# Optimization experiments

Hardware: AMD Instinct MI355X
Metric: run time of the kernel (lower is better)

The kernel has to match this reference:

```python
import jax, jax.numpy as jnp
import numpy as np

B, C, W, F, NC = 512, 12, 4, 512, 4  # batch, leads, windows(=4, hardcoded by conv0), features, classes


def setup_inputs() -> dict:
    key = jax.random.key(0)
    ks = jax.random.split(key, 16)
    g = lambda i, shape, s=1.0: jax.random.normal(ks[i], shape, jnp.float32) * s
    return {
        "x": g(0, (B, C, W, F)),
        # GRU (PyTorch layout: W_ih [3F,F], W_hh [3F,F], gate order r,z,n)
        "gru_wih": g(1, (3 * F, F), 0.03),
        "gru_whh": g(2, (3 * F, F), 0.03),
        "gru_bih": jnp.zeros((3 * F,), jnp.float32),
        "gru_bhh": jnp.zeros((3 * F,), jnp.float32),
        # GraphLearning 1x1 convs (squeezed kernels); positive biases keep adj nondegenerate
        "conv0_w": g(3, (W,), 0.5), "conv0_b": jnp.float32(0.1),
        "conv1_w": g(4, (F,), 0.05), "conv1_b": jnp.float32(0.1),
        "conv2_w": g(5, (C * C, C), 0.3),
        "conv2_b": 0.1 + 0.05 * jnp.abs(g(6, (C * C,))),
        # GCN stack
        "gcn_w": g(7, (2, F, F), 0.04), "gcn_b": jnp.zeros((2, F), jnp.float32),
        # classifier head (jax [in,out] layout); BN in eval mode
        "fc1_w": g(8, (C * F, 512), 0.02), "fc1_b": jnp.zeros((512,), jnp.float32),
        "bn1_g": jnp.ones((512,), jnp.float32), "bn1_b": jnp.zeros((512,), jnp.float32),
        "bn1_m": 0.1 * g(9, (512,)), "bn1_v": 1.0 + 0.1 * jnp.abs(g(10, (512,))),
        "fc2_w": g(11, (512, 512), 0.04), "fc2_b": jnp.zeros((512,), jnp.float32),
        "bn2_g": jnp.ones((512,), jnp.float32), "bn2_b": jnp.zeros((512,), jnp.float32),
        "bn2_m": 0.1 * g(12, (512,)), "bn2_v": 1.0 + 0.1 * jnp.abs(g(13, (512,))),
        "fc3_w": g(14, (512, NC), 0.04), "fc3_b": jnp.zeros((NC,), jnp.float32),
    }


def reference(x, gru_wih, gru_whh, gru_bih, gru_bhh,
              conv0_w, conv0_b, conv1_w, conv1_b, conv2_w, conv2_b,
              gcn_w, gcn_b,
              fc1_w, fc1_b, bn1_g, bn1_b, bn1_m, bn1_v,
              fc2_w, fc2_b, bn2_g, bn2_b, bn2_m, bn2_v,
              fc3_w, fc3_b):
    b, c, w, f = x.shape
    # --- GRU over leads dim; each window slice starts from h0=0, so merge (batch, w) ---
    xs = x.transpose(0, 2, 1, 3).reshape(b * w, c, f)            # [N, C, F]
    xW = jnp.einsum('ntf,gf->ntg', xs, gru_wih) + gru_bih        # precompute input gates [N,C,3F]

    def step(h, xw_t):
        hg = h @ gru_whh.T + gru_bhh
        xr, xz, xn = jnp.split(xw_t, 3, axis=-1)
        hr, hz, hn = jnp.split(hg, 3, axis=-1)
        r = jax.nn.sigmoid(xr + hr)
        z = jax.nn.sigmoid(xz + hz)
        n = jnp.tanh(xn + r * hn)
        h = (1.0 - z) * n + z * h
        return h, h

    _, hs = jax.lax.scan(step, jnp.zeros((b * w, f), x.dtype), xW.transpose(1, 0, 2))
    gru_out = hs.transpose(1, 0, 2).reshape(b, w, c, f).transpose(0, 2, 1, 3)  # [B,C,W,F]

    # --- GraphLearning: 1x1 convs -> 12x12 adjacency -> normalized Laplacian -> Chebyshev K=4 ---
    g0 = gru_out.transpose(0, 2, 1, 3)                               # [B,W,C,F]
    y = jax.nn.relu(jnp.einsum('bwcf,w->bcf', g0, conv0_w) + conv0_b)  # [B,C,F]
    y = jax.nn.relu(jnp.einsum('bcf,f->bc', y, conv1_w) + conv1_b)     # [B,C]
    y = jax.nn.relu(jnp.einsum('bc,kc->bk', y, conv2_w) + conv2_b)     # [B,C*C]
    a = jnp.mean(y.reshape(b, c, c), axis=0)
    adj = jax.nn.relu(a)
    degree = jnp.sum(adj, axis=1)
    adj_s = 0.5 * (adj + adj.T)
    d_hat = 1.0 / (jnp.sqrt(degree) + 1e-7)
    lap = d_hat[:, None] * (jnp.diag(degree) - adj_s) * d_hat[None, :]
    L0 = jnp.zeros_like(lap)
    L1 = lap
    L2 = 2.0 * lap @ L1 - L0
    L3 = 2.0 * lap @ L2 - L1
    cheb = jnp.stack([L0, L1, L2, L3], axis=0)                       # [4,C,C]

    # --- GCN stack with residuals (dropout is identity in eval) ---
    h = gru_out.transpose(0, 2, 1, 3)[:, :, None]                    # [B,W,1,C,F]
    tmp = h
    res = h
    for i in range(gcn_w.shape[0]):
        support = jnp.einsum('bwocf,fg->bwocg', h, gcn_w[i])
        out = jnp.einsum('wij,bwojf->bwoif', cheb, support) + gcn_b[i]
        h = jax.nn.relu(out) + res
        res = h
    h = tmp + h
    h = h[:, :, 0].sum(1).reshape(b, c * f)                          # [B, C*F]

    # --- classifier head (eval-mode BN, dropout identity) ---
    def bn(v, gmm, bt, m, var):
        return (v - m) / jnp.sqrt(var + 1e-5) * gmm + bt

    h = bn(jax.nn.leaky_relu(h @ fc1_w + fc1_b, 0.01), bn1_g, bn1_b, bn1_m, bn1_v)
    h = bn(jax.nn.leaky_relu(h @ fc2_w + fc2_b, 0.01), bn2_g, bn2_b, bn2_m, bn2_v)
    return h @ fc3_w + fc3_b
```

## Files before the change

### kernel.cpp

```cpp
#include <hip/hip_runtime.h>
#include <cmath>

constexpr int Bb  = 512;
constexpr int Cc  = 12;
constexpr int Ww  = 4;
constexpr int Ff  = 512;
constexpr int Nn  = Bb * Ww;
constexpr int Gg  = 3 * Ff;
constexpr int Mx  = Nn * Cc;

typedef __attribute__((ext_vector_type(8))) short bf16x8;
typedef __attribute__((ext_vector_type(4))) float f32x4;

__device__ __forceinline__ float sigm(float v) { return 1.f / (1.f + expf(-v)); }
__device__ __forceinline__ float b2f(ushort u) { union { float f; unsigned i; } v; v.i = ((unsigned)u) << 16; return v.f; }
__device__ __forceinline__ ushort f2b(float f) {
    union { float f; unsigned i; } v; v.f = f;
    unsigned r = v.i + 0x7FFFu + ((v.i >> 16) & 1u);
    return (ushort)(r >> 16);
}
__device__ __forceinline__ void async16(const ushort* g, ushort* l) {
    __builtin_amdgcn_global_load_lds(
        (const __attribute__((address_space(1))) unsigned int*)g,
        (__attribute__((address_space(3))) unsigned int*)l, 16, 0, 0);
}

__global__ __launch_bounds__(256) void mfma_gemm(
    const ushort* __restrict__ A, const ushort* __restrict__ Bt,
    float* __restrict__ Cf, ushort* __restrict__ Cb,
    const float* __restrict__ colBias,
    int N, int K, int kLen, int MN, int gridY)
{
    __shared__ ushort As[128 * 64], Bs[128 * 64];
    const int tid = threadIdx.x;
    const int ln = tid & 63, wv = tid >> 6;
    const int l = blockIdx.x;
    const int by = l % gridY, bx = l / gridY, bz = blockIdx.y;
    const int srow = ln >> 3;
    const int kslot = (ln & 7) ^ srow;
    const int rowA0 = by * 128 + wv * 32;
    const int rowB0 = bx * 128 + wv * 32;
    const ushort* ga = A  + (long)(rowA0 + srow) * K + bz * kLen + kslot * 8;
    const ushort* gb = Bt + (long)(rowB0 + srow) * K + bz * kLen + kslot * 8;
    ushort* la = As + wv * 32 * 64;
    ushort* lb = Bs + wv * 32 * 64;
    const int rbase = (wv >> 1) * 64, cbase = (wv & 1) * 64;
    const int mrow = ln & 15, quad = ln >> 4;

    f32x4 acc[4][4] = {};

    for (int kc = 0; kc < kLen; kc += 64) {
        #pragma unroll
        for (int i = 0; i < 4; ++i) {
            async16(ga + (long)(i * 8) * K, la + i * 8 * 64);
            async16(gb + (long)(i * 8) * K, lb + i * 8 * 64);
        }
        ga += 64; gb += 64;
        __syncthreads();
        #pragma unroll
        for (int s = 0; s < 2; ++s) {
            const int sw = (((s << 2) + quad) ^ (ln & 7)) << 3;
            bf16x8 af[4], bf[4];
            #pragma unroll
            for (int i = 0; i < 4; ++i)
                af[i] = *(const bf16x8*)(As + (rbase + i * 16 + mrow) * 64 + sw);
            #pragma unroll
            for (int j = 0; j < 4; ++j)
                bf[j] = *(const bf16x8*)(Bs + (cbase + j * 16 + mrow) * 64 + sw);
            #pragma unroll
            for (int i = 0; i < 4; ++i)
                #pragma unroll
                for (int j = 0; j < 4; ++j)
                    acc[i][j] = __builtin_amdgcn_mfma_f32_16x16x32_bf16(bf[j], af[i], acc[i][j], 0, 0, 0);
        }
        __syncthreads();
    }

    const int gr0 = by * 128 + rbase + mrow;
    const int gc0 = bx * 128 + cbase + quad * 4;
    if (Cb) {
        #pragma unroll
        for (int i = 0; i < 4; ++i) {
            const long rowoff = (long)(gr0 + i * 16) * N;
            #pragma unroll
            for (int j = 0; j < 4; ++j) {
                float c0 = 0.f, c1 = 0.f, c2 = 0.f, c3 = 0.f;
                if (colBias) {
                    const float4 cb4 = *(const float4*)(colBias + gc0 + j * 16);
                    c0 = cb4.x; c1 = cb4.y; c2 = cb4.z; c3 = cb4.w;
                }
                union { ushort u[4]; uint2 v; } pk;
                pk.u[0] = f2b(acc[i][j][0] + c0);
                pk.u[1] = f2b(acc[i][j][1] + c1);
                pk.u[2] = f2b(acc[i][j][2] + c2);
                pk.u[3] = f2b(acc[i][j][3] + c3);
                *(uint2*)&Cb[rowoff + gc0 + j * 16] = pk.v;
            }
        }
    } else {
        float* Co = Cf + (long)bz * MN;
        #pragma unroll
        for (int i = 0; i < 4; ++i) {
            const long rowoff = (long)(gr0 + i * 16) * N;
            #pragma unroll
            for (int j = 0; j < 4; ++j)
                *(f32x4*)&Co[rowoff + gc0 + j * 16] = acc[i][j];
        }
    }
}

__global__ __launch_bounds__(256) void gru_fused(
    const ushort* __restrict__ hin, const ushort* __restrict__ xb,
    const ushort* __restrict__ whhB, const ushort* __restrict__ wihB,
    const float* __restrict__ bih, const float* __restrict__ bhh,
    ushort* __restrict__ hout, ushort* __restrict__ G, int t)
{
    __shared__ ushort Ah[64 * 64], Ax[64 * 64], Bh[96 * 64], Bx[96 * 64];
    const int tid = threadIdx.x, ln = tid & 63, wv = tid >> 6;
    const int mb = blockIdx.x & 31, fb = blockIdx.x >> 5;
    const int srow = ln >> 3, kslot = (ln & 7) ^ srow;
    const int mrow = ln & 15, quad = ln >> 4;
    f32x4 aH[6] = {}, aX[6] = {};
    const ushort* hrow = hin + (long)(mb * 64) * 512;

    for (int kc = 0; kc < 512; kc += 64) {
        #pragma unroll
        for (int a = 0; a < 2; ++a) {
            const int r0 = (wv * 2 + a) * 8;
            async16(hrow + (long)(r0 + srow) * 512 + kc + kslot * 8, Ah + r0 * 64);
            async16(xb + ((long)(mb * 64 + r0 + srow) * 12 + t) * 512 + kc + kslot * 8, Ax + r0 * 64);
        }
        #pragma unroll
        for (int b8 = 0; b8 < 3; ++b8) {
            const int lr0 = (wv * 3 + b8) * 8;
            const int lr = lr0 + srow;
            const int g = lr >> 5, fc = lr & 31;
            const long wr = (long)(g * 512 + fb * 32 + fc) * 512 + kc + kslot * 8;
            async16(whhB + wr, Bh + lr0 * 64);
            async16(wihB + wr, Bx + lr0 * 64);
        }
        __syncthreads();
        #pragma unroll
        for (int s = 0; s < 2; ++s) {
            const int sw = (((s << 2) + quad) ^ (ln & 7)) << 3;
            const bf16x8 ah = *(const bf16x8*)(Ah + (wv * 16 + mrow) * 64 + sw);
            const bf16x8 ax = *(const bf16x8*)(Ax + (wv * 16 + mrow) * 64 + sw);
            #pragma unroll
            for (int jt = 0; jt < 6; ++jt) {
                const bf16x8 bh = *(const bf16x8*)(Bh + (jt * 16 + mrow) * 64 + sw);
                aH[jt] = __builtin_amdgcn_mfma_f32_16x16x32_bf16(bh, ah, aH[jt], 0, 0, 0);
            }
            #pragma unroll
            for (int jt = 0; jt < 6; ++jt) {
                const bf16x8 bx2 = *(const bf16x8*)(Bx + (jt * 16 + mrow) * 64 + sw);
                aX[jt] = __builtin_amdgcn_mfma_f32_16x16x32_bf16(bx2, ax, aX[jt], 0, 0, 0);
            }
        }
        __syncthreads();
    }

    const int n = mb * 64 + wv * 16 + mrow;
    #pragma unroll
    for (int ft = 0; ft < 2; ++ft) {
        const int f0 = fb * 32 + ft * 16 + quad * 4;
        const float4 bir = *(const float4*)(bih + f0);
        const float4 biz = *(const float4*)(bih + 512 + f0);
        const float4 bin = *(const float4*)(bih + 1024 + f0);
        const float4 bhr = *(const float4*)(bhh + f0);
        const float4 bhz = *(const float4*)(bhh + 512 + f0);
        const float4 bhn = *(const float4*)(bhh + 1024 + f0);
        union { ushort u[4]; uint2 v; } hp;
        hp.v = *(const uint2*)(hin + (long)n * 512 + f0);
        const float br[4] = {bir.x + bhr.x, bir.y + bhr.y, bir.z + bhr.z, bir.w + bhr.w};
        const float bz[4] = {biz.x + bhz.x, biz.y + bhz.y, biz.z + bhz.z, biz.w + bhz.w};
        const float bn_i[4] = {bin.x, bin.y, bin.z, bin.w};
        const float bn_h[4] = {bhn.x, bhn.y, bhn.z, bhn.w};
        union { ushort u[4]; uint2 v; } o;
        #pragma unroll
        for (int r = 0; r < 4; ++r) {
            const float rr = sigm(aH[ft][r] + aX[ft][r] + br[r]);
            const float zz = sigm(aH[2 + ft][r] + aX[2 + ft][r] + bz[r]);
            const float nv = tanhf(aX[4 + ft][r] + bn_i[r] + rr * (aH[4 + ft][r] + bn_h[r]));
            o.u[r] = f2b((1.f - zz) * nv + zz * b2f(hp.u[r]));
        }
        *(uint2*)&hout[(long)n * 512 + f0] = o.v;
        *(uint2*)&G[(long)(n * 12 + t) * 512 + f0] = o.v;
    }
}

__global__ __launch_bounds__(256) void cvt_x(const float* __restrict__ x, ushort* __restrict__ xb)
{
    const int idx = blockIdx.x * 256 + threadIdx.x;
    const int m = idx >> 6, f8 = (idx & 63) << 3;
    const int n = m / 12, c = m - n * 12;
    const int b = n >> 2, w = n & 3;
    const float* src = x + (((b * 12 + c) * 4 + w) << 9) + f8;
    const float4 a = *(const float4*)src, q = *(const float4*)(src + 4);
    uint4 o;
    o.x = (unsigned)f2b(a.x) | ((unsigned)f2b(a.y) << 16);
    o.y = (unsigned)f2b(a.z) | ((unsigned)f2b(a.w) << 16);
    o.z = (unsigned)f2b(q.x) | ((unsigned)f2b(q.y) << 16);
    o.w = (unsigned)f2b(q.z) | ((unsigned)f2b(q.w) << 16);
    *(uint4*)(xb + (m << 9) + f8) = o;
}

__global__ __launch_bounds__(256) void cvt_w2(
    const float* __restrict__ wih, const float* __restrict__ whh,
    ushort* __restrict__ wihB, ushort* __restrict__ whhB)
{
    int bx = blockIdx.x;
    const float* s; ushort* d;
    if (bx < 384) { s = wih; d = wihB; } else { s = whh; d = whhB; bx -= 384; }
    const int e = (bx * 256 + threadIdx.x) << 3;
    const float4 a = *(const float4*)(s + e), q = *(const float4*)(s + e + 4);
    uint4 o;
    o.x = (unsigned)f2b(a.x) | ((unsigned)f2b(a.y) << 16);
    o.y = (unsigned)f2b(a.z) | ((unsigned)f2b(a.w) << 16);
    o.z = (unsigned)f2b(q.x) | ((unsigned)f2b(q.y) << 16);
    o.w = (unsigned)f2b(q.z) | ((unsigned)f2b(q.w) << 16);
    *(uint4*)(d + e) = o;
}

__global__ __launch_bounds__(256) void tcvt_all(
    const float* __restrict__ gcnw, const float* __restrict__ f1w, const float* __restrict__ f2w,
    ushort* __restrict__ gw0, ushort* __restrict__ gw1,
    ushort* __restrict__ f1t, ushort* __restrict__ f2t)
{
    int by = blockIdx.y;
    const float* src; ushort* dst; int R, C;
    if (by < 16)       { src = gcnw;          dst = gw0; R = 512;  C = 512; }
    else if (by < 32)  { src = gcnw + 262144; dst = gw1; R = 512;  C = 512; by -= 16; }
    else if (by < 224) { src = f1w;           dst = f1t; R = 6144; C = 512; by -= 32; }
    else               { src = f2w;           dst = f2t; R = 512;  C = 512; by -= 224; }
    __shared__ float tl[32][33];
    const int c0 = blockIdx.x * 32, r0 = by * 32;
    const int cx = threadIdx.x & 31, ry = threadIdx.x >> 5;
    #pragma unroll
    for (int k = 0; k < 4; ++k) tl[ry + k * 8][cx] = src[(long)(r0 + ry + k * 8) * C + c0 + cx];
    __syncthreads();
    #pragma unroll
    for (int k = 0; k < 4; ++k) dst[(long)(c0 + ry + k * 8) * R + r0 + cx] = f2b(tl[cx][ry + k * 8]);
}

__global__ __launch_bounds__(256) void conv01(
    const ushort* __restrict__ G, const float* __restrict__ w0, const float* __restrict__ b0,
    const float* __restrict__ w1, const float* __restrict__ b1, float* __restrict__ y2)
{
    const int row = (blockIdx.x * 256 + threadIdx.x) >> 6;
    const int lane = threadIdx.x & 63;
    const int b = row / 12, c = row - 12 * b;
    const float w00 = w0[0], w01 = w0[1], w02 = w0[2], w03 = w0[3], bb = b0[0];
    const ushort* gp = G + ((long)(b * 4) * 12 + c) * 512;
    float s = 0.f;
    for (int f = lane; f < 512; f += 64) {
        const float v = bb + b2f(gp[f]) * w00 + b2f(gp[6144 + f]) * w01
                      + b2f(gp[12288 + f]) * w02 + b2f(gp[18432 + f]) * w03;
        s += fmaxf(v, 0.f) * w1[f];
    }
    #pragma unroll
    for (int off = 32; off; off >>= 1) s += __shfl_down(s, off);
    if (lane == 0) y2[row] = fmaxf(s + b1[0], 0.f);
}

__global__ __launch_bounds__(256) void conv2_cheb(
    const float* __restrict__ y2, const float* __restrict__ w2,
    const float* __restrict__ b2, float* __restrict__ cheb)
{
    __shared__ float ys[6144];
    __shared__ float adj[144], deg[12], dhat[12], lap[144], T2[144];
    const int tid = threadIdx.x;
    for (int i = tid; i < 6144; i += 256) ys[i] = y2[i];
    __syncthreads();
    if (tid < 144) {
        float wk[12];
        #pragma unroll
        for (int c = 0; c < 12; ++c) wk[c] = w2[tid * 12 + c];
        const float bias = b2[tid];
        float s = 0.f;
        for (int b = 0; b < 512; ++b) {
            float v = bias;
            #pragma unroll
            for (int c = 0; c < 12; ++c) v += ys[b * 12 + c] * wk[c];
            s += fmaxf(v, 0.f);
        }
        adj[tid] = fmaxf(s * (1.f / 512.f), 0.f);
    }
    __syncthreads();
    if (tid < 12) {
        float s = 0.f;
        for (int j = 0; j < 12; ++j) s += adj[tid * 12 + j];
        deg[tid] = s; dhat[tid] = 1.f / (sqrtf(s) + 1e-7f);
    }
    __syncthreads();
    if (tid < 144) {
        const int i = tid / 12, j = tid % 12;
        const float as = 0.5f * (adj[i * 12 + j] + adj[j * 12 + i]);
        lap[tid] = dhat[i] * ((i == j ? deg[i] : 0.f) - as) * dhat[j];
    }
    __syncthreads();
    if (tid < 144) {
        const int i = tid / 12, j = tid % 12;
        float s = 0.f;
        for (int kk = 0; kk < 12; ++kk) s += lap[i * 12 + kk] * lap[kk * 12 + j];
        T2[tid] = 2.f * s;
    }
    __syncthreads();
    if (tid < 144) {
        const int i = tid / 12, j = tid % 12;
        float s = 0.f;
        for (int kk = 0; kk < 12; ++kk) s += lap[i * 12 + kk] * T2[kk * 12 + j];
        cheb[tid] = 0.f;
        cheb[144 + tid] = lap[tid];
        cheb[288 + tid] = T2[tid];
        cheb[432 + tid] = 2.f * s - lap[tid];
    }
}

__global__ __launch_bounds__(256) void gcn_epi1(
    const ushort* __restrict__ S, const float* __restrict__ cheb,
    const float* __restrict__ gcnb, const ushort* __restrict__ G,
    ushort* __restrict__ H1)
{
    __shared__ float ch[576];
    const int tid = threadIdx.x;
    for (int i = tid; i < 576; i += 256) ch[i] = cheb[i];
    __syncthreads();
    const int idx = blockIdx.x * 256 + tid;
    const int f = idx & 511, bc = idx >> 9;
    const int b = bc / 12, c = bc - 12 * b;
    const float bias = gcnb[f];
    #pragma unroll
    for (int w = 0; w < 4; ++w) {
        float o = bias;
        const ushort* Sr = S + ((b * 4 + w) * 12) * 512 + f;
        const float* cw = ch + w * 144 + c * 12;
        #pragma unroll
        for (int j = 0; j < 12; ++j) o += cw[j] * b2f(Sr[j * 512]);
        const int gi = ((b * 4 + w) * 12 + c) * 512 + f;
        H1[gi] = f2b(fmaxf(o, 0.f) + b2f(G[gi]));
    }
}

__global__ __launch_bounds__(256) void gcn_epi2(
    const ushort* __restrict__ S, const float* __restrict__ cheb,
    const float* __restrict__ gcnb, const ushort* __restrict__ G,
    const ushort* __restrict__ H1, ushort* __restrict__ pooled)
{
    __shared__ float ch[576];
    const int tid = threadIdx.x;
    for (int i = tid; i < 576; i += 256) ch[i] = cheb[i];
    __syncthreads();
    const int idx = blockIdx.x * 256 + tid;
    const int f = idx & 511, bc = idx >> 9;
    const int b = bc / 12, c = bc - 12 * b;
    const float bias = gcnb[f];
    float acc = 0.f;
    #pragma unroll
    for (int w = 0; w < 4; ++w) {
        float o = bias;
        const ushort* Sr = S + ((b * 4 + w) * 12) * 512 + f;
        const float* cw = ch + w * 144 + c * 12;
        #pragma unroll
        for (int j = 0; j < 12; ++j) o += cw[j] * b2f(Sr[j * 512]);
        const int gi = ((b * 4 + w) * 12 + c) * 512 + f;
        acc += fmaxf(o, 0.f) + b2f(H1[gi]) + b2f(G[gi]);
    }
    pooled[idx] = f2b(acc);
}

__global__ __launch_bounds__(256) void fc_epi(
    const float* __restrict__ part, int nsplit, const float* __restrict__ bias,
    const float* __restrict__ g, const float* __restrict__ be,
    const float* __restrict__ mu, const float* __restrict__ var,
    ushort* __restrict__ outb, float* __restrict__ outf)
{
    const int idx = blockIdx.x * 256 + threadIdx.x;
    const int c = idx & 511;
    float s = bias[c];
    for (int k = 0; k < nsplit; ++k) s += part[k * 262144 + idx];
    s = s >= 0.f ? s : 0.01f * s;
    s = (s - mu[c]) * rsqrtf(var[c] + 1e-5f) * g[c] + be[c];
    if (outb) outb[idx] = f2b(s); else outf[idx] = s;
}

__global__ __launch_bounds__(256) void fc3_kernel(
    const float* __restrict__ z2, const float* __restrict__ w3,
    const float* __restrict__ b3, float* __restrict__ out)
{
    const int idx = blockIdx.x * 256 + threadIdx.x;
    const int m = idx >> 2, nc = idx & 3;
    float s = b3[nc];
    const float* zr = z2 + m * 512;
    for (int k = 0; k < 512; ++k) s += zr[k] * w3[k * 4 + nc];
    out[idx] = s;
}

extern "C" void kernel_launch(void* const* d_in, const int* in_sizes, int n_in,
                              void* d_out, int out_size, void* d_ws, size_t ws_size,
                              hipStream_t stream)
{
    (void)in_sizes; (void)n_in; (void)out_size; (void)ws_size;
    const float* x    = (const float*)d_in[0];
    const float* wih  = (const float*)d_in[1];
    const float* whh  = (const float*)d_in[2];
    const float* bih  = (const float*)d_in[3];
    const float* bhh  = (const float*)d_in[4];
    const float* c0w  = (const float*)d_in[5];
    const float* c0b  = (const float*)d_in[6];
    const float* c1w  = (const float*)d_in[7];
    const float* c1b  = (const float*)d_in[8];
    const float* c2w  = (const float*)d_in[9];
    const float* c2b  = (const float*)d_in[10];
    const float* gcnw = (const float*)d_in[11];
    const float* gcnb = (const float*)d_in[12];
    const float* f1w  = (const float*)d_in[13];
    const float* f1b  = (const float*)d_in[14];
    const float* bn1g = (const float*)d_in[15];
    const float* bn1b = (const float*)d_in[16];
    const float* bn1m = (const float*)d_in[17];
    const float* bn1v = (const float*)d_in[18];
    const float* f2w  = (const float*)d_in[19];
    const float* f2b_ = (const float*)d_in[20];
    const float* bn2g = (const float*)d_in[21];
    const float* bn2b = (const float*)d_in[22];
    const float* bn2m = (const float*)d_in[23];
    const float* bn2v = (const float*)d_in[24];
    const float* f3w  = (const float*)d_in[25];
    const float* f3b  = (const float*)d_in[26];

    char* W = (char*)d_ws;
    ushort* xb     = (ushort*)(W + 0);
    ushort* pooled = (ushort*)(W + 0);
    float*  z1p    = (float*)(W + 8388608);
    float*  z2p    = z1p;
    ushort* G      = (ushort*)(W + 25165824);
    ushort* S      = (ushort*)(W + 50331648);
    ushort* H1     = (ushort*)(W + 75497472);
    ushort* h0     = (ushort*)(W + 100663296);
    ushort* h1     = (ushort*)(W + 102760448);
    ushort* wihB   = (ushort*)(W + 104857600);
    ushort* whhB   = (ushort*)(W + 106430464);
    ushort* gw0    = (ushort*)(W + 108003328);
    ushort* gw1    = (ushort*)(W + 108527616);
    ushort* f1t    = (ushort*)(W + 109051904);
    ushort* f2t    = (ushort*)(W + 115343360);
    ushort* z1b    = (ushort*)(W + 115867648);
    float*  z2     = (float*)(W + 116391936);
    float*  y2     = (float*)(W + 117440512);
    float*  chebb  = (float*)(W + 117465088);

    hipMemsetAsync(h0, 0, (size_t)Nn * Ff * sizeof(ushort), stream);
    cvt_x<<<(Mx * 64) / 256, 256, 0, stream>>>(x, xb);
    cvt_w2<<<768, 256, 0, stream>>>(wih, whh, wihB, whhB);
    tcvt_all<<<dim3(16, 240), 256, 0, stream>>>(gcnw, f1w, f2w, gw0, gw1, f1t, f2t);

    ushort* hp = h0; ushort* hq = h1;
    for (int t = 0; t < Cc; ++t) {
        gru_fused<<<512, 256, 0, stream>>>(hp, xb, whhB, wihB, bih, bhh, hq, G, t);
        ushort* tmp = hp; hp = hq; hq = tmp;
    }

    conv01<<<(Bb * Cc * 64) / 256, 256, 0, stream>>>(G, c0w, c0b, c1w, c1b, y2);
    conv2_cheb<<<1, 256, 0, stream>>>(y2, c2w, c2b, chebb);

    mfma_gemm<<<dim3(768, 1), 256, 0, stream>>>(
        G, gw0, nullptr, S, nullptr, Ff, Ff, Ff, 0, 192);
    gcn_epi1<<<(Bb * Cc * Ff) / 256, 256, 0, stream>>>(S, chebb, gcnb, G, H1);

    mfma_gemm<<<dim3(768, 1), 256, 0, stream>>>(
        H1, gw1, nullptr, S, nullptr, Ff, Ff, Ff, 0, 192);
    gcn_epi2<<<(Bb * Cc * Ff) / 256, 256, 0, stream>>>(S, chebb, gcnb + Ff, G, H1, pooled);

    mfma_gemm<<<dim3(16, 16), 256, 0, stream>>>(
        pooled, f1t, z1p, nullptr, nullptr, 512, Cc * Ff, 384, 262144, 4);
    fc_epi<<<1024, 256, 0, stream>>>(z1p, 16, f1b, bn1g, bn1b, bn1m, bn1v, z1b, nullptr);
    mfma_gemm<<<dim3(16, 4), 256, 0, stream>>>(
        z1b, f2t, z2p, nullptr, nullptr, 512, 512, 128, 262144, 4);
    fc_epi<<<1024, 256, 0, stream>>>(z2p, 4, f2b_, bn2g, bn2b, bn2m, bn2v, nullptr, z2);
    fc3_kernel<<<(Bb * 4) / 256, 256, 0, stream>>>(z2, f3w, f3b, (float*)d_out);
}
```

Measured before the change: 493.5 us.

## Merge prep kernels, fuse conv stages, skip h-path at t=0, remap GRU blocks

Combines the three conversion/transpose kernels into one launch and drops the h0 memset. The first GRU step now skips the hidden-state GEMM and the h loads, since h0 is zero. conv01 and conv2_cheb are fused using an atomic ticket so the last block computes the Chebyshev matrices. GRU block indices are remapped so neighbouring blocks share weight tiles, and the unused colBias path is removed from the GEMM. Together these cut launch count and redundant work, at the cost of a grid-level atomic and a reliance on zeroed sync counters.

```diff
diff --git a/kernel.cpp b/kernel.cpp
--- a/kernel.cpp
+++ b/kernel.cpp
@@ -28,7 +28,6 @@
 __global__ __launch_bounds__(256) void mfma_gemm(
     const ushort* __restrict__ A, const ushort* __restrict__ Bt,
     float* __restrict__ Cf, ushort* __restrict__ Cb,
-    const float* __restrict__ colBias,
     int N, int K, int kLen, int MN, int gridY)
 {
     __shared__ ushort As[128 * 64], Bs[128 * 64];
@@ -38,10 +37,8 @@
     const int by = l % gridY, bx = l / gridY, bz = blockIdx.y;
     const int srow = ln >> 3;
     const int kslot = (ln & 7) ^ srow;
-    const int rowA0 = by * 128 + wv * 32;
-    const int rowB0 = bx * 128 + wv * 32;
-    const ushort* ga = A  + (long)(rowA0 + srow) * K + bz * kLen + kslot * 8;
-    const ushort* gb = Bt + (long)(rowB0 + srow) * K + bz * kLen + kslot * 8;
+    const ushort* ga = A  + (long)(by * 128 + wv * 32 + srow) * K + bz * kLen + kslot * 8;
+    const ushort* gb = Bt + (long)(bx * 128 + wv * 32 + srow) * K + bz * kLen + kslot * 8;
     ushort* la = As + wv * 32 * 64;
     ushort* lb = Bs + wv * 32 * 64;
     const int rbase = (wv >> 1) * 64, cbase = (wv & 1) * 64;
@@ -84,16 +81,9 @@
             const long rowoff = (long)(gr0 + i * 16) * N;
             #pragma unroll
             for (int j = 0; j < 4; ++j) {
-                float c0 = 0.f, c1 = 0.f, c2 = 0.f, c3 = 0.f;
-                if (colBias) {
-                    const float4 cb4 = *(const float4*)(colBias + gc0 + j * 16);
-                    c0 = cb4.x; c1 = cb4.y; c2 = cb4.z; c3 = cb4.w;
-                }
                 union { ushort u[4]; uint2 v; } pk;
-                pk.u[0] = f2b(acc[i][j][0] + c0);
-                pk.u[1] = f2b(acc[i][j][1] + c1);
-                pk.u[2] = f2b(acc[i][j][2] + c2);
-                pk.u[3] = f2b(acc[i][j][3] + c3);
+                pk.u[0] = f2b(acc[i][j][0]); pk.u[1] = f2b(acc[i][j][1]);
+                pk.u[2] = f2b(acc[i][j][2]); pk.u[3] = f2b(acc[i][j][3]);
                 *(uint2*)&Cb[rowoff + gc0 + j * 16] = pk.v;
             }
         }
@@ -117,9 +107,12 @@
 {
     __shared__ ushort Ah[64 * 64], Ax[64 * 64], Bh[96 * 64], Bx[96 * 64];
     const int tid = threadIdx.x, ln = tid & 63, wv = tid >> 6;
-    const int mb = blockIdx.x & 31, fb = blockIdx.x >> 5;
+    const int p = blockIdx.x;
+    const int fb = ((p & 7) << 1) | (p >> 8);
+    const int mb = (p >> 3) & 31;
     const int srow = ln >> 3, kslot = (ln & 7) ^ srow;
     const int mrow = ln & 15, quad = ln >> 4;
+    const int th = (t != 0);
     f32x4 aH[6] = {}, aX[6] = {};
     const ushort* hrow = hin + (long)(mb * 64) * 512;
 
@@ -127,7 +120,7 @@
         #pragma unroll
         for (int a = 0; a < 2; ++a) {
             const int r0 = (wv * 2 + a) * 8;
-            async16(hrow + (long)(r0 + srow) * 512 + kc + kslot * 8, Ah + r0 * 64);
+            if (th) async16(hrow + (long)(r0 + srow) * 512 + kc + kslot * 8, Ah + r0 * 64);
             async16(xb + ((long)(mb * 64 + r0 + srow) * 12 + t) * 512 + kc + kslot * 8, Ax + r0 * 64);
         }
         #pragma unroll
@@ -136,24 +129,26 @@
             const int lr = lr0 + srow;
             const int g = lr >> 5, fc = lr & 31;
             const long wr = (long)(g * 512 + fb * 32 + fc) * 512 + kc + kslot * 8;
-            async16(whhB + wr, Bh + lr0 * 64);
+            if (th) async16(whhB + wr, Bh + lr0 * 64);
             async16(wihB + wr, Bx + lr0 * 64);
         }
         __syncthreads();
         #pragma unroll
         for (int s = 0; s < 2; ++s) {
             const int sw = (((s << 2) + quad) ^ (ln & 7)) << 3;
-            const bf16x8 ah = *(const bf16x8*)(Ah + (wv * 16 + mrow) * 64 + sw);
             const bf16x8 ax = *(const bf16x8*)(Ax + (wv * 16 + mrow) * 64 + sw);
-            #pragma unroll
-            for (int jt = 0; jt < 6; ++jt) {
-                const bf16x8 bh = *(const bf16x8*)(Bh + (jt * 16 + mrow) * 64 + sw);
-                aH[jt] = __builtin_amdgcn_mfma_f32_16x16x32_bf16(bh, ah, aH[jt], 0, 0, 0);
-            }
             #pragma unroll
             for (int jt = 0; jt < 6; ++jt) {
                 const bf16x8 bx2 = *(const bf16x8*)(Bx + (jt * 16 + mrow) * 64 + sw);
                 aX[jt] = __builtin_amdgcn_mfma_f32_16x16x32_bf16(bx2, ax, aX[jt], 0, 0, 0);
+            }
+            if (th) {
+                const bf16x8 ah = *(const bf16x8*)(Ah + (wv * 16 + mrow) * 64 + sw);
+                #pragma unroll
+                for (int jt = 0; jt < 6; ++jt) {
+                    const bf16x8 bh = *(const bf16x8*)(Bh + (jt * 16 + mrow) * 64 + sw);
+                    aH[jt] = __builtin_amdgcn_mfma_f32_16x16x32_bf16(bh, ah, aH[jt], 0, 0, 0);
+                }
             }
         }
         __syncthreads();
@@ -169,106 +164,114 @@
         const float4 bhr = *(const float4*)(bhh + f0);
         const float4 bhz = *(const float4*)(bhh + 512 + f0);
         const float4 bhn = *(const float4*)(bhh + 1024 + f0);
-        union { ushort u[4]; uint2 v; } hp;
-        hp.v = *(const uint2*)(hin + (long)n * 512 + f0);
         const float br[4] = {bir.x + bhr.x, bir.y + bhr.y, bir.z + bhr.z, bir.w + bhr.w};
         const float bz[4] = {biz.x + bhz.x, biz.y + bhz.y, biz.z + bhz.z, biz.w + bhz.w};
-        const float bn_i[4] = {bin.x, bin.y, bin.z, bin.w};
-        const float bn_h[4] = {bhn.x, bhn.y, bhn.z, bhn.w};
+        const float bnI[4] = {bin.x, bin.y, bin.z, bin.w};
+        const float bnH[4] = {bhn.x, bhn.y, bhn.z, bhn.w};
+        union { ushort u[4]; uint2 v; } hpk;
+        if (th) hpk.v = *(const uint2*)(hin + (long)n * 512 + f0);
         union { ushort u[4]; uint2 v; } o;
         #pragma unroll
         for (int r = 0; r < 4; ++r) {
+            const float hprev = th ? b2f(hpk.u[r]) : 0.f;
             const float rr = sigm(aH[ft][r] + aX[ft][r] + br[r]);
             const float zz = sigm(aH[2 + ft][r] + aX[2 + ft][r] + bz[r]);
-            const float nv = tanhf(aX[4 + ft][r] + bn_i[r] + rr * (aH[4 + ft][r] + bn_h[r]));
-            o.u[r] = f2b((1.f - zz) * nv + zz * b2f(hp.u[r]));
+            const float nv = tanhf(aX[4 + ft][r] + bnI[r] + rr * (aH[4 + ft][r] + bnH[r]));
+            o.u[r] = f2b((1.f - zz) * nv + zz * hprev);
         }
         *(uint2*)&hout[(long)n * 512 + f0] = o.v;
         *(uint2*)&G[(long)(n * 12 + t) * 512 + f0] = o.v;
     }
 }
 
-__global__ __launch_bounds__(256) void cvt_x(const float* __restrict__ x, ushort* __restrict__ xb)
-{
-    const int idx = blockIdx.x * 256 + threadIdx.x;
-    const int m = idx >> 6, f8 = (idx & 63) << 3;
-    const int n = m / 12, c = m - n * 12;
-    const int b = n >> 2, w = n & 3;
-    const float* src = x + (((b * 12 + c) * 4 + w) << 9) + f8;
-    const float4 a = *(const float4*)src, q = *(const float4*)(src + 4);
-    uint4 o;
-    o.x = (unsigned)f2b(a.x) | ((unsigned)f2b(a.y) << 16);
-    o.y = (unsigned)f2b(a.z) | ((unsigned)f2b(a.w) << 16);
-    o.z = (unsigned)f2b(q.x) | ((unsigned)f2b(q.y) << 16);
-    o.w = (unsigned)f2b(q.z) | ((unsigned)f2b(q.w) << 16);
-    *(uint4*)(xb + (m << 9) + f8) = o;
-}
-
-__global__ __launch_bounds__(256) void cvt_w2(
+__global__ __launch_bounds__(256) void prep_all(
+    const float* __restrict__ x, ushort* __restrict__ xb,
     const float* __restrict__ wih, const float* __restrict__ whh,
-    ushort* __restrict__ wihB, ushort* __restrict__ whhB)
-{
-    int bx = blockIdx.x;
-    const float* s; ushort* d;
-    if (bx < 384) { s = wih; d = wihB; } else { s = whh; d = whhB; bx -= 384; }
-    const int e = (bx * 256 + threadIdx.x) << 3;
-    const float4 a = *(const float4*)(s + e), q = *(const float4*)(s + e + 4);
-    uint4 o;
-    o.x = (unsigned)f2b(a.x) | ((unsigned)f2b(a.y) << 16);
-    o.y = (unsigned)f2b(a.z) | ((unsigned)f2b(a.w) << 16);
-    o.z = (unsigned)f2b(q.x) | ((unsigned)f2b(q.y) << 16);
-    o.w = (unsigned)f2b(q.z) | ((unsigned)f2b(q.w) << 16);
-    *(uint4*)(d + e) = o;
-}
-
-__global__ __launch_bounds__(256) void tcvt_all(
+    ushort* __restrict__ wihB, ushort* __restrict__ whhB,
     const float* __restrict__ gcnw, const float* __restrict__ f1w, const float* __restrict__ f2w,
     ushort* __restrict__ gw0, ushort* __restrict__ gw1,
-    ushort* __restrict__ f1t, ushort* __restrict__ f2t)
-{
-    int by = blockIdx.y;
-    const float* src; ushort* dst; int R, C;
-    if (by < 16)       { src = gcnw;          dst = gw0; R = 512;  C = 512; }
-    else if (by < 32)  { src = gcnw + 262144; dst = gw1; R = 512;  C = 512; by -= 16; }
-    else if (by < 224) { src = f1w;           dst = f1t; R = 6144; C = 512; by -= 32; }
-    else               { src = f2w;           dst = f2t; R = 512;  C = 512; by -= 224; }
+    ushort* __restrict__ f1t, ushort* __restrict__ f2t,
+    unsigned* __restrict__ sync)
+{
     __shared__ float tl[32][33];
-    const int c0 = blockIdx.x * 32, r0 = by * 32;
-    const int cx = threadIdx.x & 31, ry = threadIdx.x >> 5;
-    #pragma unroll
-    for (int k = 0; k < 4; ++k) tl[ry + k * 8][cx] = src[(long)(r0 + ry + k * 8) * C + c0 + cx];
-    __syncthreads();
-    #pragma unroll
-    for (int k = 0; k < 4; ++k) dst[(long)(c0 + ry + k * 8) * R + r0 + cx] = f2b(tl[cx][ry + k * 8]);
-}
-
-__global__ __launch_bounds__(256) void conv01(
+    const int bx = blockIdx.x, tid = threadIdx.x;
+    if (bx == 0 && tid < 16) sync[tid] = 0;
+    if (bx < 6144) {
+        const int idx = bx * 256 + tid;
+        const int m = idx >> 6, f8 = (idx & 63) << 3;
+        const int n = m / 12, c = m - n * 12;
+        const int b = n >> 2, w = n & 3;
+        const float* src = x + (((b * 12 + c) * 4 + w) << 9) + f8;
+        const float4 a = *(const float4*)src, q = *(const float4*)(src + 4);
+        uint4 o;
+        o.x = (unsigned)f2b(a.x) | ((unsigned)f2b(a.y) << 16);
+        o.y = (unsigned)f2b(a.z) | ((unsigned)f2b(a.w) << 16);
+        o.z = (unsigned)f2b(q.x) | ((unsigned)f2b(q.y) << 16);
+        o.w = (unsigned)f2b(q.z) | ((unsigned)f2b(q.w) << 16);
+        *(uint4*)(xb + (m << 9) + f8) = o;
+    } else if (bx < 6912) {
+        int b2 = bx - 6144;
+        const float* s; ushort* d;
+        if (b2 < 384) { s = wih; d = wihB; } else { s = whh; d = whhB; b2 -= 384; }
+        const int e = (b2 * 256 + tid) << 3;
+        const float4 a = *(const float4*)(s + e), q = *(const float4*)(s + e + 4);
+        uint4 o;
+        o.x = (unsigned)f2b(a.x) | ((unsigned)f2b(a.y) << 16);
+        o.y = (unsigned)f2b(a.z) | ((unsigned)f2b(a.w) << 16);
+        o.z = (unsigned)f2b(q.x) | ((unsigned)f2b(q.y) << 16);
+        o.w = (unsigned)f2b(q.z) | ((unsigned)f2b(q.w) << 16);
+        *(uint4*)(d + e) = o;
+    } else {
+        int idx = bx - 6912;
+        const int tx = idx & 15;
+        int by = idx >> 4;
+        const float* src; ushort* dst; int R, C;
+        if (by < 16)       { src = gcnw;          dst = gw0; R = 512;  C = 512; }
+        else if (by < 32)  { src = gcnw + 262144; dst = gw1; R = 512;  C = 512; by -= 16; }
+        else if (by < 224) { src = f1w;           dst = f1t; R = 6144; C = 512; by -= 32; }
+        else               { src = f2w;           dst = f2t; R = 512;  C = 512; by -= 224; }
+        const int c0 = tx * 32, r0 = by * 32;
+        const int cx = tid & 31, ry = tid >> 5;
+        #pragma unroll
+        for (int k = 0; k < 4; ++k) tl[ry + k * 8][cx] = src[(long)(r0 + ry + k * 8) * C + c0 + cx];
+        __syncthreads();
+        #pragma unroll
+        for (int k = 0; k < 4; ++k) dst[(long)(c0 + ry + k * 8) * R + r0 + cx] = f2b(tl[cx][ry + k * 8]);
+    }
+}
+
+__global__ __launch_bounds__(256) void conv01_cheb(
     const ushort* __restrict__ G, const float* __restrict__ w0, const float* __restrict__ b0,
-    const float* __restrict__ w1, const float* __restrict__ b1, float* __restrict__ y2)
-{
-    const int row = (blockIdx.x * 256 + threadIdx.x) >> 6;
-    const int lane = threadIdx.x & 63;
-    const int b = row / 12, c = row - 12 * b;
-    const float w00 = w0[0], w01 = w0[1], w02 = w0[2], w03 = w0[3], bb = b0[0];
-    const ushort* gp = G + ((long)(b * 4) * 12 + c) * 512;
-    float s = 0.f;
-    for (int f = lane; f < 512; f += 64) {
-        const float v = bb + b2f(gp[f]) * w00 + b2f(gp[6144 + f]) * w01
-                      + b2f(gp[12288 + f]) * w02 + b2f(gp[18432 + f]) * w03;
-        s += fmaxf(v, 0.f) * w1[f];
-    }
-    #pragma unroll
-    for (int off = 32; off; off >>= 1) s += __shfl_down(s, off);
-    if (lane == 0) y2[row] = fmaxf(s + b1[0], 0.f);
-}
-
-__global__ __launch_bounds__(256) void conv2_cheb(
-    const float* __restrict__ y2, const float* __restrict__ w2,
-    const float* __restrict__ b2, float* __restrict__ cheb)
-{
+    const float* __restrict__ w1, const float* __restrict__ b1,
+    const float* __restrict__ w2, const float* __restrict__ b2,
+    float* __restrict__ y2, float* __restrict__ cheb, unsigned* __restrict__ done)
+{
+    const int tid = threadIdx.x;
+    {
+        const int row = (blockIdx.x * 256 + tid) >> 6;
+        const int lane = tid & 63;
+        const int b = row / 12, c = row - 12 * b;
+        const float w00 = w0[0], w01 = w0[1], w02 = w0[2], w03 = w0[3], bb = b0[0];
+        const ushort* gp = G + ((long)(b * 4) * 12 + c) * 512;
+        float s = 0.f;
+        for (int f = lane; f < 512; f += 64) {
+            const float v = bb + b2f(gp[f]) * w00 + b2f(gp[6144 + f]) * w01
+                          + b2f(gp[12288 + f]) * w02 + b2f(gp[18432 + f]) * w03;
+            s += fmaxf(v, 0.f) * w1[f];
+        }
+        #pragma unroll
+        for (int off = 32; off; off >>= 1) s += __shfl_down(s, off);
+        if (lane == 0) y2[row] = fmaxf(s + b1[0], 0.f);
+    }
+    __syncthreads();
+    __shared__ unsigned ticket;
+    if (tid == 0)
+        ticket = __hip_atomic_fetch_add(done, 1u, __ATOMIC_ACQ_REL, __HIP_MEMORY_SCOPE_AGENT);
+    __syncthreads();
+    if (ticket != gridDim.x - 1) return;
+
     __shared__ float ys[6144];
     __shared__ float adj[144], deg[12], dhat[12], lap[144], T2[144];
-    const int tid = threadIdx.x;
     for (int i = tid; i < 6144; i += 256) ys[i] = y2[i];
     __syncthreads();
     if (tid < 144) {
@@ -448,11 +451,10 @@
     float*  z2     = (float*)(W + 116391936);
     float*  y2     = (float*)(W + 117440512);
     float*  chebb  = (float*)(W + 117465088);
-
-    hipMemsetAsync(h0, 0, (size_t)Nn * Ff * sizeof(ushort), stream);
-    cvt_x<<<(Mx * 64) / 256, 256, 0, stream>>>(x, xb);
-    cvt_w2<<<768, 256, 0, stream>>>(wih, whh, wihB, whhB);
-    tcvt_all<<<dim3(16, 240), 256, 0, stream>>>(gcnw, f1w, f2w, gw0, gw1, f1t, f2t);
+    unsigned* sync = (unsigned*)(W + 117469184);
+
+    prep_all<<<10752, 256, 0, stream>>>(x, xb, wih, whh, wihB, whhB,
+                                        gcnw, f1w, f2w, gw0, gw1, f1t, f2t, sync);
 
     ushort* hp = h0; ushort* hq = h1;
     for (int t = 0; t < Cc; ++t) {
@@ -460,22 +462,22 @@
         ushort* tmp = hp; hp = hq; hq = tmp;
     }
 
-    conv01<<<(Bb * Cc * 64) / 256, 256, 0, stream>>>(G, c0w, c0b, c1w, c1b, y2);
-    conv2_cheb<<<1, 256, 0, stream>>>(y2, c2w, c2b, chebb);
+    conv01_cheb<<<(Bb * Cc * 64) / 256, 256, 0, stream>>>(
+        G, c0w, c0b, c1w, c1b, c2w, c2b, y2, chebb, sync + 12);
 
     mfma_gemm<<<dim3(768, 1), 256, 0, stream>>>(
-        G, gw0, nullptr, S, nullptr, Ff, Ff, Ff, 0, 192);
+        G, gw0, nullptr, S, Ff, Ff, Ff, 0, 192);
     gcn_epi1<<<(Bb * Cc * Ff) / 256, 256, 0, stream>>>(S, chebb, gcnb, G, H1);
 
     mfma_gemm<<<dim3(768, 1), 256, 0, stream>>>(
-        H1, gw1, nullptr, S, nullptr, Ff, Ff, Ff, 0, 192);
+        H1, gw1, nullptr, S, Ff, Ff, Ff, 0, 192);
     gcn_epi2<<<(Bb * Cc * Ff) / 256, 256, 0, stream>>>(S, chebb, gcnb + Ff, G, H1, pooled);
 
     mfma_gemm<<<dim3(16, 16), 256, 0, stream>>>(
-        pooled, f1t, z1p, nullptr, nullptr, 512, Cc * Ff, 384, 262144, 4);
+        pooled, f1t, z1p, nullptr, 512, Cc * Ff, 384, 262144, 4);
     fc_epi<<<1024, 256, 0, stream>>>(z1p, 16, f1b, bn1g, bn1b, bn1m, bn1v, z1b, nullptr);
     mfma_gemm<<<dim3(16, 4), 256, 0, stream>>>(
-        z1b, f2t, z2p, nullptr, nullptr, 512, 512, 128, 262144, 4);
+        z1b, f2t, z2p, nullptr, 512, 512, 128, 262144, 4);
     fc_epi<<<1024, 256, 0, stream>>>(z2p, 4, f2b_, bn2g, bn2b, bn2m, bn2v, nullptr, z2);
     fc3_kernel<<<(Bb * 4) / 256, 256, 0, stream>>>(z2, f3w, f3b, (float*)d_out);
 }
```

Measured after the change: 579.9 us. 1.18x slower.
